# Kernel optimization log

Hardware: AMD Instinct MI355X
Metric: run time of the kernel (lower is better)

The kernel has to match this reference:

```python
import jax, jax.numpy as jnp
import numpy as np

EPS = 1e-5  # torch nn.LayerNorm default eps


def setup_inputs() -> dict:
    key = jax.random.key(0)
    k1, k2 = jax.random.split(key)
    dim = 1024
    x = jax.random.normal(k1, (8, 4096, dim), dtype=jnp.float32)
    ln_gamma = jnp.ones((dim,), dtype=jnp.float32)
    ln_beta = jnp.zeros((dim,), dtype=jnp.float32)
    # Linear(dim, 2*dim): stored here as [in, out] for x @ W
    W = jax.random.normal(k2, (dim, 2 * dim), dtype=jnp.float32) * (1.0 / np.sqrt(dim))
    b = jnp.zeros((2 * dim,), dtype=jnp.float32)
    return {"x": x, "ln_gamma": ln_gamma, "ln_beta": ln_beta, "W": W, "b": b}


def reference(x, ln_gamma, ln_beta, W, b):
    # LayerNorm over last dim
    mu = jnp.mean(x, axis=-1, keepdims=True)
    var = jnp.mean(jnp.square(x - mu), axis=-1, keepdims=True)
    h = (x - mu) * jax.lax.rsqrt(var + EPS) * ln_gamma + ln_beta
    # Gated linear: project to 2*dim, chunk into value/gate
    proj = jnp.einsum('bsd,de->bse', h, W) + b  # [B,S,2*dim]
    v, g = jnp.split(proj, 2, axis=-1)
    # Dropout is identity in eval mode; residual add
    return x + v * jax.nn.sigmoid(g)
```

## Files before the change

### kernel.cpp

```cpp
#include <hip/hip_runtime.h>
#include <cstdint>

typedef short bf16x8 __attribute__((ext_vector_type(8)));
typedef float f32x4  __attribute__((ext_vector_type(4)));

#define DIM   1024
#define NROWS 32768

__device__ __forceinline__ ushort f2bf(float f){
  union { float f; uint32_t u; } v; v.f = f;
  uint32_t u = v.u;
  return (ushort)((u + 0x7fffu + ((u >> 16) & 1u)) >> 16);
}

__global__ void ln_kernel(const float* __restrict__ x,
                          const float* __restrict__ gamma,
                          const float* __restrict__ beta,
                          ushort* __restrict__ h){
  const int w = threadIdx.x >> 6;
  const int l = threadIdx.x & 63;
  const int row = blockIdx.x * 4 + w;
  const float4* xr = (const float4*)(x + (size_t)row * DIM);
  float4 v[4];
  float s = 0.f, ss = 0.f;
#pragma unroll
  for (int i = 0; i < 4; ++i){
    v[i] = xr[i * 64 + l];
    s  += v[i].x + v[i].y + v[i].z + v[i].w;
    ss += v[i].x * v[i].x + v[i].y * v[i].y + v[i].z * v[i].z + v[i].w * v[i].w;
  }
#pragma unroll
  for (int m = 1; m < 64; m <<= 1){
    s  += __shfl_xor(s,  m, 64);
    ss += __shfl_xor(ss, m, 64);
  }
  const float mean = s * (1.f / 1024.f);
  const float var  = ss * (1.f / 1024.f) - mean * mean;
  const float rstd = rsqrtf(var + 1e-5f);
  ushort* hr = h + (size_t)row * DIM;
#pragma unroll
  for (int i = 0; i < 4; ++i){
    const int c = (i * 64 + l) * 4;
    float4 gm = ((const float4*)gamma)[i * 64 + l];
    float4 bt = ((const float4*)beta )[i * 64 + l];
    ushort4 o;
    o.x = f2bf((v[i].x - mean) * rstd * gm.x + bt.x);
    o.y = f2bf((v[i].y - mean) * rstd * gm.y + bt.y);
    o.z = f2bf((v[i].z - mean) * rstd * gm.z + bt.z);
    o.w = f2bf((v[i].w - mean) * rstd * gm.w + bt.w);
    *(ushort4*)(hr + c) = o;
  }
}

__global__ void wt_kernel(const float* __restrict__ W, ushort* __restrict__ Wt){
  __shared__ float tile[64][65];
  const int t  = threadIdx.x;
  const int k0 = blockIdx.x * 64;
  const int n0 = blockIdx.y * 64;
  const int lr = t >> 4;
  const int lc = (t & 15) * 4;
#pragma unroll
  for (int p = 0; p < 4; ++p){
    const int kk = p * 16 + lr;
    float4 val = *(const float4*)(W + (size_t)(k0 + kk) * 2048 + n0 + lc);
    tile[kk][lc + 0] = val.x; tile[kk][lc + 1] = val.y;
    tile[kk][lc + 2] = val.z; tile[kk][lc + 3] = val.w;
  }
  __syncthreads();
#pragma unroll
  for (int p = 0; p < 4; ++p){
    const int nn = p * 16 + lr;
    ushort4 o;
    o.x = f2bf(tile[lc + 0][nn]);
    o.y = f2bf(tile[lc + 1][nn]);
    o.z = f2bf(tile[lc + 2][nn]);
    o.w = f2bf(tile[lc + 3][nn]);
    *(ushort4*)(Wt + (size_t)(n0 + nn) * 1024 + k0 + lc) = o;
  }
}

__global__ __launch_bounds__(256)
void glu_gemm(const ushort* __restrict__ hA,
              const ushort* __restrict__ Wt,
              const float*  __restrict__ bias,
              const float*  __restrict__ x,
              float* __restrict__ out){
  __shared__ ushort As[128][64];
  __shared__ ushort Bs[128][64];

  const int w = threadIdx.x >> 6;
  const int l = threadIdx.x & 63;
  const int brow  = blockIdx.x * 128;
  const int ncol0 = blockIdx.y * 64;

  f32x4 acc[2][8];
  const f32x4 zero = {0.f, 0.f, 0.f, 0.f};
#pragma unroll
  for (int i = 0; i < 2; ++i)
#pragma unroll
    for (int j = 0; j < 8; ++j) acc[i][j] = zero;

  const int lr8 = l >> 3;
  const int lc8 = (l & 7) * 8;

  for (int kt = 0; kt < 16; ++kt){
    const int k0 = kt * 64;
#pragma unroll
    for (int i = 0; i < 4; ++i){
      const int rbase = i * 32 + w * 8;
      const ushort* gp = hA + (size_t)(brow + rbase + lr8) * 1024 + k0 + lc8;
      __builtin_amdgcn_global_load_lds((const __attribute__((address_space(1))) void*)gp,
                                       (__attribute__((address_space(3))) void*)&As[rbase][0],
                                       16, 0, 0);
    }
#pragma unroll
    for (int i = 0; i < 4; ++i){
      const int rbase = i * 32 + w * 8;
      const int tt = rbase + lr8;
      const int wrow = ncol0 + tt + ((tt >> 6) * 960);
      const ushort* gp = Wt + (size_t)wrow * 1024 + k0 + lc8;
      __builtin_amdgcn_global_load_lds((const __attribute__((address_space(1))) void*)gp,
                                       (__attribute__((address_space(3))) void*)&Bs[rbase][0],
                                       16, 0, 0);
    }
    __syncthreads();
#pragma unroll
    for (int ks = 0; ks < 2; ++ks){
      bf16x8 a[2], b[8];
      const int ko = ks * 32 + ((l >> 4) << 3);
#pragma unroll
      for (int mi = 0; mi < 2; ++mi)
        a[mi] = *(const bf16x8*)&As[w * 32 + mi * 16 + (l & 15)][ko];
#pragma unroll
      for (int ni = 0; ni < 8; ++ni)
        b[ni] = *(const bf16x8*)&Bs[ni * 16 + (l & 15)][ko];
#pragma unroll
      for (int mi = 0; mi < 2; ++mi)
#pragma unroll
        for (int ni = 0; ni < 8; ++ni)
          acc[mi][ni] = __builtin_amdgcn_mfma_f32_16x16x32_bf16(a[mi], b[ni], acc[mi][ni], 0, 0, 0);
    }
    __syncthreads();
  }

  float bv[4], bg[4];
#pragma unroll
  for (int ni = 0; ni < 4; ++ni){
    const int col = ncol0 + ni * 16 + (l & 15);
    bv[ni] = bias[col];
    bg[ni] = bias[col + 1024];
  }
  const int rb = brow + w * 32 + ((l >> 4) << 2);
#pragma unroll
  for (int mi = 0; mi < 2; ++mi){
#pragma unroll
    for (int r = 0; r < 4; ++r){
      const int row = rb + mi * 16 + r;
      const float* xrow = x   + (size_t)row * 1024;
      float*       orow = out + (size_t)row * 1024;
#pragma unroll
      for (int ni = 0; ni < 4; ++ni){
        const int col = ncol0 + ni * 16 + (l & 15);
        const float vv = acc[mi][ni    ][r] + bv[ni];
        const float gg = acc[mi][ni + 4][r] + bg[ni];
        const float sg = 1.f / (1.f + __expf(-gg));
        orow[col] = xrow[col] + vv * sg;
      }
    }
  }
}

extern "C" void kernel_launch(void* const* d_in, const int* in_sizes, int n_in,
                              void* d_out, int out_size, void* d_ws, size_t ws_size,
                              hipStream_t stream){
  const float* x     = (const float*)d_in[0];
  const float* gamma = (const float*)d_in[1];
  const float* beta  = (const float*)d_in[2];
  const float* W     = (const float*)d_in[3];
  const float* b     = (const float*)d_in[4];
  float* out = (float*)d_out;

  ushort* h  = (ushort*)d_ws;
  ushort* Wt = (ushort*)((char*)d_ws + (size_t)NROWS * DIM * 2);

  ln_kernel<<<NROWS / 4, 256, 0, stream>>>(x, gamma, beta, h);
  wt_kernel<<<dim3(16, 32), 256, 0, stream>>>(W, Wt);
  glu_gemm<<<dim3(NROWS / 128, 16), 256, 0, stream>>>(h, Wt, b, x, out);
}
```

Measured before the change: 478.8 us.

## Restructure GLU GEMM with triple-buffered LDS pipeline, larger tiles, swizzle

Rewrites the GEMM kernel to use 512-thread blocks computing 128x256 output tiles (128 value + 128 gate columns), with a 3-slot LDS ring buffer that prefetches two k-tiles ahead using async global-to-LDS loads and fine-grained vmcnt waits. LDS columns are XOR-swizzled to avoid bank conflicts, block IDs are remapped for L2 locality, and setprio wraps the MFMA phases. The aim is to overlap memory latency with matrix math and raise reuse per loaded tile. In exchange it needs much more LDS and more registers per block, which may limit occupancy.

```diff
diff --git a/kernel.cpp b/kernel.cpp
--- a/kernel.cpp
+++ b/kernel.cpp
@@ -79,90 +79,153 @@
   }
 }
 
-__global__ __launch_bounds__(256)
+#define SLOT_U   24576
+#define B_OFF    8192
+
+__global__ __launch_bounds__(512, 2)
 void glu_gemm(const ushort* __restrict__ hA,
               const ushort* __restrict__ Wt,
               const float*  __restrict__ bias,
               const float*  __restrict__ x,
               float* __restrict__ out){
-  __shared__ ushort As[128][64];
-  __shared__ ushort Bs[128][64];
-
-  const int w = threadIdx.x >> 6;
-  const int l = threadIdx.x & 63;
-  const int brow  = blockIdx.x * 128;
-  const int ncol0 = blockIdx.y * 64;
-
-  f32x4 acc[2][8];
+  __shared__ ushort smem[3 * SLOT_U];
+
+  const int tid = threadIdx.x;
+  const int l   = tid & 63;
+  const int w   = tid >> 6;
+  const int wm  = w >> 2;
+  const int wn  = w & 3;
+
+  const int bid = blockIdx.x;
+  const int sw  = (bid & 7) * 256 + (bid >> 3);
+  const int bm  = sw >> 3;
+  const int bn  = sw & 7;
+  const int brow  = bm * 128;
+  const int ncol0 = bn * 128;
+
+  const int rg = tid >> 3;
+  const int c  = tid & 7;
+
+  auto stageA = [&](int kt, int slot){
+    const int k0 = kt * 64;
+#pragma unroll
+    for (int i = 0; i < 2; ++i){
+      const int r = i * 64 + rg;
+      const ushort* gp = hA + (size_t)(brow + r) * 1024 + k0 + ((c ^ (r & 7)) * 8);
+      ushort* lp = &smem[slot * SLOT_U + (i * 64 + w * 8) * 64];
+      __builtin_amdgcn_global_load_lds((const __attribute__((address_space(1))) void*)gp,
+                                       (__attribute__((address_space(3))) void*)lp, 16, 0, 0);
+    }
+  };
+  auto stageB = [&](int kt, int slot, int j){
+    const int k0 = kt * 64;
+    const int tB = j * 64 + rg;
+    const int wrow = ncol0 + (tB & 127) + ((tB >> 7) * 1024);
+    const ushort* gp = Wt + (size_t)wrow * 1024 + k0 + ((c ^ (tB & 7)) * 8);
+    ushort* lp = &smem[slot * SLOT_U + B_OFF + (j * 64 + w * 8) * 64];
+    __builtin_amdgcn_global_load_lds((const __attribute__((address_space(1))) void*)gp,
+                                     (__attribute__((address_space(3))) void*)lp, 16, 0, 0);
+  };
+
+  auto readA = [&](int slot, int m, int kk) -> bf16x8 {
+    const int R  = wm * 64 + m * 16 + (l & 15);
+    const int pc = (kk * 4 + (l >> 4)) ^ (l & 7);
+    return *(const bf16x8*)&smem[slot * SLOT_U + R * 64 + pc * 8];
+  };
+  auto readB = [&](int slot, int nf, int kk) -> bf16x8 {
+    const int Br = (nf >> 1) * 128 + wn * 32 + (nf & 1) * 16 + (l & 15);
+    const int pc = (kk * 4 + (l >> 4)) ^ (l & 7);
+    return *(const bf16x8*)&smem[slot * SLOT_U + B_OFF + Br * 64 + pc * 8];
+  };
+
+  f32x4 acc[4][4];
   const f32x4 zero = {0.f, 0.f, 0.f, 0.f};
 #pragma unroll
-  for (int i = 0; i < 2; ++i)
-#pragma unroll
-    for (int j = 0; j < 8; ++j) acc[i][j] = zero;
-
-  const int lr8 = l >> 3;
-  const int lc8 = (l & 7) * 8;
-
+  for (int i = 0; i < 4; ++i)
+#pragma unroll
+    for (int j = 0; j < 4; ++j) acc[i][j] = zero;
+
+  stageA(0, 0);
+#pragma unroll
+  for (int j = 0; j < 4; ++j) stageB(0, 0, j);
+  stageA(1, 1);
+#pragma unroll
+  for (int j = 0; j < 4; ++j) stageB(1, 1, j);
+  asm volatile("s_waitcnt vmcnt(6)" ::: "memory");
+  __builtin_amdgcn_s_barrier();
+  __builtin_amdgcn_sched_barrier(0);
+
+#pragma unroll
   for (int kt = 0; kt < 16; ++kt){
-    const int k0 = kt * 64;
-#pragma unroll
-    for (int i = 0; i < 4; ++i){
-      const int rbase = i * 32 + w * 8;
-      const ushort* gp = hA + (size_t)(brow + rbase + lr8) * 1024 + k0 + lc8;
-      __builtin_amdgcn_global_load_lds((const __attribute__((address_space(1))) void*)gp,
-                                       (__attribute__((address_space(3))) void*)&As[rbase][0],
-                                       16, 0, 0);
+    const int slot  = kt % 3;
+    const int pslot = (kt + 2) % 3;
+    const bool do_stage = (kt < 14);
+
+    bf16x8 bfr[4][2], a0[2][2];
+#pragma unroll
+    for (int nf = 0; nf < 4; ++nf)
+#pragma unroll
+      for (int kk = 0; kk < 2; ++kk) bfr[nf][kk] = readB(slot, nf, kk);
+#pragma unroll
+    for (int m = 0; m < 2; ++m)
+#pragma unroll
+      for (int kk = 0; kk < 2; ++kk) a0[m][kk] = readA(slot, m, kk);
+    if (do_stage){ stageA(kt + 2, pslot); stageB(kt + 2, pslot, 0); }
+    __builtin_amdgcn_s_setprio(1);
+#pragma unroll
+    for (int m = 0; m < 2; ++m)
+#pragma unroll
+      for (int nf = 0; nf < 4; ++nf)
+#pragma unroll
+        for (int kk = 0; kk < 2; ++kk)
+          acc[m][nf] = __builtin_amdgcn_mfma_f32_16x16x32_bf16(a0[m][kk], bfr[nf][kk], acc[m][nf], 0, 0, 0);
+    __builtin_amdgcn_s_setprio(0);
+
+    bf16x8 a1[2][2];
+#pragma unroll
+    for (int m = 0; m < 2; ++m)
+#pragma unroll
+      for (int kk = 0; kk < 2; ++kk) a1[m][kk] = readA(slot, m + 2, kk);
+    if (do_stage){ stageB(kt + 2, pslot, 1); stageB(kt + 2, pslot, 2); stageB(kt + 2, pslot, 3); }
+    __builtin_amdgcn_s_setprio(1);
+#pragma unroll
+    for (int m = 0; m < 2; ++m)
+#pragma unroll
+      for (int nf = 0; nf < 4; ++nf)
+#pragma unroll
+        for (int kk = 0; kk < 2; ++kk)
+          acc[m + 2][nf] = __builtin_amdgcn_mfma_f32_16x16x32_bf16(a1[m][kk], bfr[nf][kk], acc[m + 2][nf], 0, 0, 0);
+    __builtin_amdgcn_s_setprio(0);
+
+    if (kt < 15){
+      __builtin_amdgcn_sched_barrier(0);
+      if (kt < 14) asm volatile("s_waitcnt vmcnt(6)" ::: "memory");
+      else         asm volatile("s_waitcnt vmcnt(0)" ::: "memory");
+      __builtin_amdgcn_s_barrier();
+      __builtin_amdgcn_sched_barrier(0);
     }
-#pragma unroll
-    for (int i = 0; i < 4; ++i){
-      const int rbase = i * 32 + w * 8;
-      const int tt = rbase + lr8;
-      const int wrow = ncol0 + tt + ((tt >> 6) * 960);
-      const ushort* gp = Wt + (size_t)wrow * 1024 + k0 + lc8;
-      __builtin_amdgcn_global_load_lds((const __attribute__((address_space(1))) void*)gp,
-                                       (__attribute__((address_space(3))) void*)&Bs[rbase][0],
-                                       16, 0, 0);
-    }
-    __syncthreads();
-#pragma unroll
-    for (int ks = 0; ks < 2; ++ks){
-      bf16x8 a[2], b[8];
-      const int ko = ks * 32 + ((l >> 4) << 3);
-#pragma unroll
-      for (int mi = 0; mi < 2; ++mi)
-        a[mi] = *(const bf16x8*)&As[w * 32 + mi * 16 + (l & 15)][ko];
-#pragma unroll
-      for (int ni = 0; ni < 8; ++ni)
-        b[ni] = *(const bf16x8*)&Bs[ni * 16 + (l & 15)][ko];
-#pragma unroll
-      for (int mi = 0; mi < 2; ++mi)
-#pragma unroll
-        for (int ni = 0; ni < 8; ++ni)
-          acc[mi][ni] = __builtin_amdgcn_mfma_f32_16x16x32_bf16(a[mi], b[ni], acc[mi][ni], 0, 0, 0);
-    }
-    __syncthreads();
-  }
-
-  float bv[4], bg[4];
-#pragma unroll
-  for (int ni = 0; ni < 4; ++ni){
-    const int col = ncol0 + ni * 16 + (l & 15);
-    bv[ni] = bias[col];
-    bg[ni] = bias[col + 1024];
-  }
-  const int rb = brow + w * 32 + ((l >> 4) << 2);
-#pragma unroll
-  for (int mi = 0; mi < 2; ++mi){
+  }
+
+  float bv[2], bg[2];
+#pragma unroll
+  for (int n = 0; n < 2; ++n){
+    const int col = ncol0 + wn * 32 + n * 16 + (l & 15);
+    bv[n] = bias[col];
+    bg[n] = bias[col + 1024];
+  }
+  const int rb = brow + wm * 64 + ((l >> 4) << 2);
+#pragma unroll
+  for (int m = 0; m < 4; ++m){
 #pragma unroll
     for (int r = 0; r < 4; ++r){
-      const int row = rb + mi * 16 + r;
+      const int row = rb + m * 16 + r;
       const float* xrow = x   + (size_t)row * 1024;
       float*       orow = out + (size_t)row * 1024;
 #pragma unroll
-      for (int ni = 0; ni < 4; ++ni){
-        const int col = ncol0 + ni * 16 + (l & 15);
-        const float vv = acc[mi][ni    ][r] + bv[ni];
-        const float gg = acc[mi][ni + 4][r] + bg[ni];
+      for (int n = 0; n < 2; ++n){
+        const int col = ncol0 + wn * 32 + n * 16 + (l & 15);
+        const float vv = acc[m][n    ][r] + bv[n];
+        const float gg = acc[m][n + 2][r] + bg[n];
         const float sg = 1.f / (1.f + __expf(-gg));
         orow[col] = xrow[col] + vv * sg;
       }
@@ -185,5 +248,5 @@
 
   ln_kernel<<<NROWS / 4, 256, 0, stream>>>(x, gamma, beta, h);
   wt_kernel<<<dim3(16, 32), 256, 0, stream>>>(W, Wt);
-  glu_gemm<<<dim3(NROWS / 128, 16), 256, 0, stream>>>(h, Wt, b, x, out);
-}
+  glu_gemm<<<2048, 512, 0, stream>>>(h, Wt, b, x, out);
+}
```

New measurement: 390.0 us. -18.5%, faster.
